# Performance work log

Hardware: AMD Instinct MI355X
Metric: run time of the kernel (lower is better)

## Reference

```python
import jax, jax.numpy as jnp
import numpy as np

# DenoiseTransform(h=10, template_window_size=7, search_window_size=21)
KS = 7                 # odd template window -> kernel_size (7, 7)
SIGMA_COLOR = 10.0     # float(h)
SIGMA_SPACE = 21.0     # float(search_window_size), same for y and x


def _gauss1d(ks, sigma):
    # kornia.get_gaussian_kernel1d: centered, normalized to sum 1
    x = jnp.arange(ks, dtype=jnp.float32) - ks // 2
    g = jnp.exp(-0.5 * (x / sigma) ** 2)
    return g / g.sum()


def setup_inputs() -> dict:
    key = jax.random.key(0)
    # batch of 8 RGB 512x512 images in [0, 1]
    img = jax.random.uniform(key, (8, 3, 512, 512), dtype=jnp.float32)
    return {"img": img}


def reference(img):
    """kornia.filters.bilateral_blur(img, (7,7), 10.0, (21.0,21.0)),
    border_type='reflect', color_distance_type='l1'.
    Fused over the 7x7 window: never materializes (B,C,H,W,49)."""
    ks = KS
    pad = ks // 2
    space = jnp.outer(_gauss1d(ks, SIGMA_SPACE), _gauss1d(ks, SIGMA_SPACE))  # (ks, ks)
    B, C, H, W = img.shape
    padded = jnp.pad(img, ((0, 0), (0, 0), (pad, pad), (pad, pad)), mode="reflect")
    num = jnp.zeros_like(img)                      # (B, C, H, W)
    den = jnp.zeros((B, 1, H, W), dtype=img.dtype)  # (B, 1, H, W)
    neg_half_inv_sc2 = -0.5 / (SIGMA_COLOR ** 2)
    for i in range(ks):          # fixed small 7x7 window -> static unrolled loop
        for j in range(ks):
            patch = jax.lax.dynamic_slice(padded, (0, 0, i, j), (B, C, H, W))
            # L1 color distance over channels, then squared (kornia default 'l1')
            d = jnp.abs(patch - img).sum(axis=1, keepdims=True)  # (B,1,H,W)
            w = space[i, j] * jnp.exp(neg_half_inv_sc2 * d * d)   # (B,1,H,W)
            num = num + w * patch
            den = den + w
    return num / den
```

## Files before the change

### kernel.cpp

```cpp
#include <hip/hip_runtime.h>

#define BB 8
#define HH 512
#define WW 512
#define HW (HH * WW)

typedef float f32x2 __attribute__((ext_vector_type(2)));

__device__ __forceinline__ int reflect512(int v) {
    v = v < 0 ? -v : v;
    return v >= 512 ? 1022 - v : v;
}

__device__ __forceinline__ float swx(int dx) {
    const float SW[7] = {0.98984784f, 0.99547514f, 0.99886688f, 1.0f,
                         0.99886688f, 0.99547514f, 0.98984784f};
    return (dx < -3 || dx > 3) ? 0.0f : SW[dx + 3];
}

#define C1S (-5.0e-3f)
#define C2S (1.25e-5f)

__global__ __launch_bounds__(256) void bilateral_pk2(const float* __restrict__ in,
                                                     float* __restrict__ out) {
    const int blk = blockIdx.x;
    if (blk < BB * HH) {
        const int b = blk >> 9;
        const int y = blk & 511;
        const int p = threadIdx.x;
        if (p >= 253) return;
        const int e  = 4 + 2 * p;
        const int xb = e - 4;

        const float* __restrict__ p0 = in + (size_t)(3 * b) * HW;
        const float* __restrict__ p1 = p0 + HW;
        const float* __restrict__ p2 = p1 + HW;

        const int crow = y * WW;
        f32x2 m0 = *(const f32x2*)(p0 + crow + e - 2);
        f32x2 m1 = *(const f32x2*)(p1 + crow + e - 2);
        f32x2 m2 = *(const f32x2*)(p2 + crow + e - 2);
        f32x2 g0 = *(const f32x2*)(p0 + crow + e);
        f32x2 g1 = *(const f32x2*)(p1 + crow + e);
        f32x2 g2 = *(const f32x2*)(p2 + crow + e);
        const float cA0 = m0.y, cA1 = m1.y, cA2 = m2.y;
        const float cB0 = g0.x, cB1 = g1.x, cB2 = g2.x;

        f32x2 aA0 = {0.f,0.f}, aA1 = {0.f,0.f}, aA2 = {0.f,0.f}, aAd = {0.f,0.f};
        f32x2 aB0 = {0.f,0.f}, aB1 = {0.f,0.f}, aB2 = {0.f,0.f}, aBd = {0.f,0.f};

        const f32x2 C1v = {C1S, C1S};
        const f32x2 C2v = {C2S, C2S};
        const f32x2 ONE = {1.0f, 1.0f};

        #pragma unroll
        for (int j = 0; j < 7; ++j) {
            const float wj = swx(j - 3);
            const int rb = reflect512(y - 3 + j) * WW + xb;
            const float* r0 = p0 + rb;
            const float* r1 = p1 + rb;
            const float* r2 = p2 + rb;
            #pragma unroll
            for (int i = 0; i < 4; ++i) {
                f32x2 q0 = *(const f32x2*)(r0 + 2 * i);
                f32x2 q1 = *(const f32x2*)(r1 + 2 * i);
                f32x2 q2 = *(const f32x2*)(r2 + 2 * i);
                {
                    float dlo = fabsf(q0.x-cA0) + fabsf(q1.x-cA1) + fabsf(q2.x-cA2);
                    float dhi = fabsf(q0.y-cA0) + fabsf(q1.y-cA1) + fabsf(q2.y-cA2);
                    f32x2 dp = {dlo, dhi};
                    f32x2 d2 = dp * dp;
                    const f32x2 sc = {wj * swx(2*i-3), wj * swx(2*i-2)};
                    f32x2 t = C2v * d2 + C1v;
                    f32x2 w = (t * d2 + ONE) * sc;
                    aA0 += w * q0; aA1 += w * q1; aA2 += w * q2; aAd += w;
                }
                {
                    float dlo = fabsf(q0.x-cB0) + fabsf(q1.x-cB1) + fabsf(q2.x-cB2);
                    float dhi = fabsf(q0.y-cB0) + fabsf(q1.y-cB1) + fabsf(q2.y-cB2);
                    f32x2 dp = {dlo, dhi};
                    f32x2 d2 = dp * dp;
                    const f32x2 sc = {wj * swx(2*i-4), wj * swx(2*i-3)};
                    f32x2 t = C2v * d2 + C1v;
                    f32x2 w = (t * d2 + ONE) * sc;
                    aB0 += w * q0; aB1 += w * q1; aB2 += w * q2; aBd += w;
                }
            }
        }

        const float iA = 1.0f / (aAd.x + aAd.y);
        const float iB = 1.0f / (aBd.x + aBd.y);
        size_t ob = (size_t)(3 * b) * HW + crow;
        out[ob + e - 1]          = (aA0.x + aA0.y) * iA;
        out[ob + HW + e - 1]     = (aA1.x + aA1.y) * iA;
        out[ob + 2 * HW + e - 1] = (aA2.x + aA2.y) * iA;
        out[ob + e]              = (aB0.x + aB0.y) * iB;
        out[ob + HW + e]         = (aB1.x + aB1.y) * iB;
        out[ob + 2 * HW + e]     = (aB2.x + aB2.y) * iB;
    } else {
        int idx  = (blk - BB * HH) * 256 + threadIdx.x;
        int ci   = idx % 6;
        int rest = idx / 6;
        int y = rest & 511;
        int b = rest >> 9;
        int x = ci < 3 ? ci : 506 + ci;

        const float* __restrict__ p0 = in + (size_t)(3 * b) * HW;
        const float* __restrict__ p1 = p0 + HW;
        const float* __restrict__ p2 = p1 + HW;
        int cidx = y * WW + x;
        float c0 = p0[cidx], c1 = p1[cidx], c2 = p2[cidx];
        float n0 = 0.f, n1 = 0.f, n2 = 0.f, dn = 0.f;
        #pragma unroll
        for (int dy = 0; dy < 7; ++dy) {
            int rbase = reflect512(y + dy - 3) * WW;
            float wy = swx(dy - 3);
            #pragma unroll
            for (int dx = 0; dx < 7; ++dx) {
                int o = rbase + reflect512(x + dx - 3);
                float q0 = p0[o], q1 = p1[o], q2 = p2[o];
                float d  = fabsf(q0 - c0) + fabsf(q1 - c1) + fabsf(q2 - c2);
                float d2 = d * d;
                float w  = wy * swx(dx - 3) * fmaf(fmaf(C2S, d2, C1S), d2, 1.0f);
                n0 += w * q0; n1 += w * q1; n2 += w * q2; dn += w;
            }
        }
        float inv = 1.0f / dn;
        size_t ob = (size_t)(3 * b) * HW + cidx;
        out[ob] = n0 * inv; out[ob + HW] = n1 * inv; out[ob + 2 * HW] = n2 * inv;
    }
}

extern "C" void kernel_launch(void* const* d_in, const int* in_sizes, int n_in,
                              void* d_out, int out_size, void* d_ws, size_t ws_size,
                              hipStream_t stream) {
    const float* in = (const float*)d_in[0];
    float* out = (float*)d_out;
    int blocks = BB * HH + (BB * HH * 6) / 256;
    bilateral_pk2<<<blocks, 256, 0, stream>>>(in, out);
}
```

Before: 51.04 us.

## Compute two output rows per thread with register row reuse and block swizzle

Each thread now produces a 2x2 output quad (two rows, two columns), so the 8 input rows loaded through a double-buffered register window serve both output rows instead of reloading 7 rows per row. Blocks shrink to 128 threads, each covering half a row-pair, and block indices are swizzled across batches. This cuts global/L2 load traffic per output. In exchange it roughly doubles accumulator register use, which may lower occupancy.

```diff
diff --git a/kernel.cpp b/kernel.cpp
--- a/kernel.cpp
+++ b/kernel.cpp
@@ -21,84 +21,121 @@
 #define C1S (-5.0e-3f)
 #define C2S (1.25e-5f)
 
-__global__ __launch_bounds__(256) void bilateral_pk2(const float* __restrict__ in,
-                                                     float* __restrict__ out) {
+__global__ __launch_bounds__(128) void bilateral_quad(const float* __restrict__ in,
+                                                      float* __restrict__ out) {
     const int blk = blockIdx.x;
-    if (blk < BB * HH) {
-        const int b = blk >> 9;
-        const int y = blk & 511;
-        const int p = threadIdx.x;
-        if (p >= 253) return;
-        const int e  = 4 + 2 * p;
+    if (blk < 4096) {
+        const int swz  = (blk & 7) * 512 + (blk >> 3);
+        const int b    = swz >> 9;
+        const int rest = swz & 511;
+        const int y0   = (rest >> 1) * 2;
+        const int h    = rest & 1;
+        const int p    = threadIdx.x;
+        const int nact = h ? 126 : 127;
+        if (p >= nact) return;
+        const int e  = 4 + 254 * h + 2 * p;
         const int xb = e - 4;
 
         const float* __restrict__ p0 = in + (size_t)(3 * b) * HW;
         const float* __restrict__ p1 = p0 + HW;
         const float* __restrict__ p2 = p1 + HW;
 
-        const int crow = y * WW;
-        f32x2 m0 = *(const f32x2*)(p0 + crow + e - 2);
-        f32x2 m1 = *(const f32x2*)(p1 + crow + e - 2);
-        f32x2 m2 = *(const f32x2*)(p2 + crow + e - 2);
-        f32x2 g0 = *(const f32x2*)(p0 + crow + e);
-        f32x2 g1 = *(const f32x2*)(p1 + crow + e);
-        f32x2 g2 = *(const f32x2*)(p2 + crow + e);
-        const float cA0 = m0.y, cA1 = m1.y, cA2 = m2.y;
-        const float cB0 = g0.x, cB1 = g1.x, cB2 = g2.x;
+        float cA[2][3], cB[2][3];
+        #pragma unroll
+        for (int row = 0; row < 2; ++row) {
+            const int rb = (y0 + row) * WW + xb;
+            f32x2 m0 = *(const f32x2*)(p0 + rb + 2);
+            f32x2 m1 = *(const f32x2*)(p1 + rb + 2);
+            f32x2 m2 = *(const f32x2*)(p2 + rb + 2);
+            f32x2 g0 = *(const f32x2*)(p0 + rb + 4);
+            f32x2 g1 = *(const f32x2*)(p1 + rb + 4);
+            f32x2 g2 = *(const f32x2*)(p2 + rb + 4);
+            cA[row][0] = m0.y; cA[row][1] = m1.y; cA[row][2] = m2.y;
+            cB[row][0] = g0.x; cB[row][1] = g1.x; cB[row][2] = g2.x;
+        }
 
-        f32x2 aA0 = {0.f,0.f}, aA1 = {0.f,0.f}, aA2 = {0.f,0.f}, aAd = {0.f,0.f};
-        f32x2 aB0 = {0.f,0.f}, aB1 = {0.f,0.f}, aB2 = {0.f,0.f}, aBd = {0.f,0.f};
+        f32x2 aN0[2][2], aN1[2][2], aN2[2][2], aD[2][2];
+        #pragma unroll
+        for (int row = 0; row < 2; ++row)
+            #pragma unroll
+            for (int a = 0; a < 2; ++a) {
+                aN0[row][a] = (f32x2){0.f, 0.f}; aN1[row][a] = (f32x2){0.f, 0.f};
+                aN2[row][a] = (f32x2){0.f, 0.f}; aD[row][a]  = (f32x2){0.f, 0.f};
+            }
 
-        const f32x2 C1v = {C1S, C1S};
-        const f32x2 C2v = {C2S, C2S};
-        const f32x2 ONE = {1.0f, 1.0f};
+        f32x2 q0[2][4], q1[2][4], q2[2][4];
+        {
+            const int rb = reflect512(y0 - 3) * WW + xb;
+            #pragma unroll
+            for (int i = 0; i < 4; ++i) {
+                q0[0][i] = *(const f32x2*)(p0 + rb + 2 * i);
+                q1[0][i] = *(const f32x2*)(p1 + rb + 2 * i);
+                q2[0][i] = *(const f32x2*)(p2 + rb + 2 * i);
+            }
+        }
+
+        const f32x2 C1v = {C1S, C1S}, C2v = {C2S, C2S}, ONE = {1.f, 1.f};
 
         #pragma unroll
-        for (int j = 0; j < 7; ++j) {
-            const float wj = swx(j - 3);
-            const int rb = reflect512(y - 3 + j) * WW + xb;
-            const float* r0 = p0 + rb;
-            const float* r1 = p1 + rb;
-            const float* r2 = p2 + rb;
+        for (int r = 0; r < 8; ++r) {
+            const int cur = r & 1, nx = cur ^ 1;
+            if (r < 7) {
+                const int rb = reflect512(y0 - 2 + r) * WW + xb;
+                #pragma unroll
+                for (int i = 0; i < 4; ++i) {
+                    q0[nx][i] = *(const f32x2*)(p0 + rb + 2 * i);
+                    q1[nx][i] = *(const f32x2*)(p1 + rb + 2 * i);
+                    q2[nx][i] = *(const f32x2*)(p2 + rb + 2 * i);
+                }
+            }
             #pragma unroll
             for (int i = 0; i < 4; ++i) {
-                f32x2 q0 = *(const f32x2*)(r0 + 2 * i);
-                f32x2 q1 = *(const f32x2*)(r1 + 2 * i);
-                f32x2 q2 = *(const f32x2*)(r2 + 2 * i);
-                {
-                    float dlo = fabsf(q0.x-cA0) + fabsf(q1.x-cA1) + fabsf(q2.x-cA2);
-                    float dhi = fabsf(q0.y-cA0) + fabsf(q1.y-cA1) + fabsf(q2.y-cA2);
-                    f32x2 dp = {dlo, dhi};
-                    f32x2 d2 = dp * dp;
-                    const f32x2 sc = {wj * swx(2*i-3), wj * swx(2*i-2)};
-                    f32x2 t = C2v * d2 + C1v;
-                    f32x2 w = (t * d2 + ONE) * sc;
-                    aA0 += w * q0; aA1 += w * q1; aA2 += w * q2; aAd += w;
-                }
-                {
-                    float dlo = fabsf(q0.x-cB0) + fabsf(q1.x-cB1) + fabsf(q2.x-cB2);
-                    float dhi = fabsf(q0.y-cB0) + fabsf(q1.y-cB1) + fabsf(q2.y-cB2);
-                    f32x2 dp = {dlo, dhi};
-                    f32x2 d2 = dp * dp;
-                    const f32x2 sc = {wj * swx(2*i-4), wj * swx(2*i-3)};
-                    f32x2 t = C2v * d2 + C1v;
-                    f32x2 w = (t * d2 + ONE) * sc;
-                    aB0 += w * q0; aB1 += w * q1; aB2 += w * q2; aBd += w;
+                const f32x2 v0 = q0[cur][i], v1 = q1[cur][i], v2 = q2[cur][i];
+                #pragma unroll
+                for (int row = 0; row < 2; ++row) {
+                    const int dy = r - row;
+                    if (dy < 0 || dy > 6) continue;
+                    const float wj = swx(dy - 3);
+                    {
+                        float dlo = fabsf(v0.x-cA[row][0]) + fabsf(v1.x-cA[row][1]) + fabsf(v2.x-cA[row][2]);
+                        float dhi = fabsf(v0.y-cA[row][0]) + fabsf(v1.y-cA[row][1]) + fabsf(v2.y-cA[row][2]);
+                        f32x2 dp = {dlo, dhi};
+                        f32x2 d2 = dp * dp;
+                        const f32x2 sc = {wj * swx(2*i-3), wj * swx(2*i-2)};
+                        f32x2 t = C2v * d2 + C1v;
+                        f32x2 w = (t * d2 + ONE) * sc;
+                        aN0[row][0] += w * v0; aN1[row][0] += w * v1;
+                        aN2[row][0] += w * v2; aD[row][0] += w;
+                    }
+                    {
+                        float dlo = fabsf(v0.x-cB[row][0]) + fabsf(v1.x-cB[row][1]) + fabsf(v2.x-cB[row][2]);
+                        float dhi = fabsf(v0.y-cB[row][0]) + fabsf(v1.y-cB[row][1]) + fabsf(v2.y-cB[row][2]);
+                        f32x2 dp = {dlo, dhi};
+                        f32x2 d2 = dp * dp;
+                        const f32x2 sc = {wj * swx(2*i-4), wj * swx(2*i-3)};
+                        f32x2 t = C2v * d2 + C1v;
+                        f32x2 w = (t * d2 + ONE) * sc;
+                        aN0[row][1] += w * v0; aN1[row][1] += w * v1;
+                        aN2[row][1] += w * v2; aD[row][1] += w;
+                    }
                 }
             }
         }
 
-        const float iA = 1.0f / (aAd.x + aAd.y);
-        const float iB = 1.0f / (aBd.x + aBd.y);
-        size_t ob = (size_t)(3 * b) * HW + crow;
-        out[ob + e - 1]          = (aA0.x + aA0.y) * iA;
-        out[ob + HW + e - 1]     = (aA1.x + aA1.y) * iA;
-        out[ob + 2 * HW + e - 1] = (aA2.x + aA2.y) * iA;
-        out[ob + e]              = (aB0.x + aB0.y) * iB;
-        out[ob + HW + e]         = (aB1.x + aB1.y) * iB;
-        out[ob + 2 * HW + e]     = (aB2.x + aB2.y) * iB;
+        #pragma unroll
+        for (int row = 0; row < 2; ++row) {
+            const float iA = 1.0f / (aD[row][0].x + aD[row][0].y);
+            const float iB = 1.0f / (aD[row][1].x + aD[row][1].y);
+            size_t ob = (size_t)(3 * b) * HW + (size_t)(y0 + row) * WW;
+            out[ob + e - 1]          = (aN0[row][0].x + aN0[row][0].y) * iA;
+            out[ob + HW + e - 1]     = (aN1[row][0].x + aN1[row][0].y) * iA;
+            out[ob + 2 * HW + e - 1] = (aN2[row][0].x + aN2[row][0].y) * iA;
+            out[ob + e]              = (aN0[row][1].x + aN0[row][1].y) * iB;
+            out[ob + HW + e]         = (aN1[row][1].x + aN1[row][1].y) * iB;
+            out[ob + 2 * HW + e]     = (aN2[row][1].x + aN2[row][1].y) * iB;
+        }
     } else {
-        int idx  = (blk - BB * HH) * 256 + threadIdx.x;
+        int idx  = (blk - 4096) * 128 + threadIdx.x;
         int ci   = idx % 6;
         int rest = idx / 6;
         int y = rest & 511;
@@ -136,6 +173,6 @@
                               hipStream_t stream) {
     const float* in = (const float*)d_in[0];
     float* out = (float*)d_out;
-    int blocks = BB * HH + (BB * HH * 6) / 256;
-    bilateral_pk2<<<blocks, 256, 0, stream>>>(in, out);
+    int blocks = 4096 + 192;
+    bilateral_quad<<<blocks, 128, 0, stream>>>(in, out);
 }
```

Result: faster. 43.28 us (-15.2%).

## Register-block 4x2 output pixels per thread with shared row loads

Applied to the files above, without the earlier changes.

Each thread now computes a 2-row by 4-column tile of output pixels. It loads 8 input rows as float4 vectors and reuses each loaded row across both output rows and all four columns, which cuts global and L1 load traffic per pixel. The spatial weight is folded into precomputed polynomial coefficients, dropping one multiply per tap. The border path now covers 4 columns on each side. The grid shrinks to 1024+128 blocks, which raises register pressure and may lower occupancy and the number of waves in flight.

```diff
diff --git a/kernel.cpp b/kernel.cpp
--- a/kernel.cpp
+++ b/kernel.cpp
@@ -6,6 +6,7 @@
 #define HW (HH * WW)
 
 typedef float f32x2 __attribute__((ext_vector_type(2)));
+typedef float f32x4 __attribute__((ext_vector_type(4)));
 
 __device__ __forceinline__ int reflect512(int v) {
     v = v < 0 ? -v : v;
@@ -21,89 +22,127 @@
 #define C1S (-5.0e-3f)
 #define C2S (1.25e-5f)
 
-__global__ __launch_bounds__(256) void bilateral_pk2(const float* __restrict__ in,
-                                                     float* __restrict__ out) {
+__global__ __launch_bounds__(256) void bilateral_q8(const float* __restrict__ in,
+                                                    float* __restrict__ out) {
     const int blk = blockIdx.x;
-    if (blk < BB * HH) {
-        const int b = blk >> 9;
-        const int y = blk & 511;
-        const int p = threadIdx.x;
-        if (p >= 253) return;
-        const int e  = 4 + 2 * p;
-        const int xb = e - 4;
+    if (blk < 1024) {
+        const int b   = blk & 7;
+        const int rp2 = blk >> 3;
+        const int sub = threadIdx.x >> 7;
+        const int c   = threadIdx.x & 127;
+        if (c == 0 || c == 127) return;
+        const int y0 = rp2 * 4 + sub * 2;
+        const int x0 = 4 * c;
+        const int xl = x0 - 4;
 
         const float* __restrict__ p0 = in + (size_t)(3 * b) * HW;
         const float* __restrict__ p1 = p0 + HW;
         const float* __restrict__ p2 = p1 + HW;
 
-        const int crow = y * WW;
-        f32x2 m0 = *(const f32x2*)(p0 + crow + e - 2);
-        f32x2 m1 = *(const f32x2*)(p1 + crow + e - 2);
-        f32x2 m2 = *(const f32x2*)(p2 + crow + e - 2);
-        f32x2 g0 = *(const f32x2*)(p0 + crow + e);
-        f32x2 g1 = *(const f32x2*)(p1 + crow + e);
-        f32x2 g2 = *(const f32x2*)(p2 + crow + e);
-        const float cA0 = m0.y, cA1 = m1.y, cA2 = m2.y;
-        const float cB0 = g0.x, cB1 = g1.x, cB2 = g2.x;
+        float cc[2][3][4];
+        #pragma unroll
+        for (int row = 0; row < 2; ++row) {
+            const int cb = (y0 + row) * WW + x0;
+            f32x4 C0 = *(const f32x4*)(p0 + cb);
+            f32x4 C1 = *(const f32x4*)(p1 + cb);
+            f32x4 C2 = *(const f32x4*)(p2 + cb);
+            cc[row][0][0]=C0.x; cc[row][0][1]=C0.y; cc[row][0][2]=C0.z; cc[row][0][3]=C0.w;
+            cc[row][1][0]=C1.x; cc[row][1][1]=C1.y; cc[row][1][2]=C1.z; cc[row][1][3]=C1.w;
+            cc[row][2][0]=C2.x; cc[row][2][1]=C2.y; cc[row][2][2]=C2.z; cc[row][2][3]=C2.w;
+        }
 
-        f32x2 aA0 = {0.f,0.f}, aA1 = {0.f,0.f}, aA2 = {0.f,0.f}, aAd = {0.f,0.f};
-        f32x2 aB0 = {0.f,0.f}, aB1 = {0.f,0.f}, aB2 = {0.f,0.f}, aBd = {0.f,0.f};
+        f32x2 acc[2][4][4];
+        #pragma unroll
+        for (int row = 0; row < 2; ++row)
+            #pragma unroll
+            for (int k = 0; k < 4; ++k)
+                #pragma unroll
+                for (int v = 0; v < 4; ++v) acc[row][k][v] = (f32x2){0.f, 0.f};
 
-        const f32x2 C1v = {C1S, C1S};
-        const f32x2 C2v = {C2S, C2S};
-        const f32x2 ONE = {1.0f, 1.0f};
+        const float SWT[7] = {0.98984784f, 0.99547514f, 0.99886688f, 1.0f,
+                              0.99886688f, 0.99547514f, 0.98984784f};
 
         #pragma unroll
-        for (int j = 0; j < 7; ++j) {
-            const float wj = swx(j - 3);
-            const int rb = reflect512(y - 3 + j) * WW + xb;
-            const float* r0 = p0 + rb;
-            const float* r1 = p1 + rb;
-            const float* r2 = p2 + rb;
+        for (int r = 0; r < 8; ++r) {
+            const int rb = reflect512(y0 - 3 + r) * WW + xl;
+            f32x4 L0a = *(const f32x4*)(p0 + rb);
+            f32x4 L0b = *(const f32x4*)(p0 + rb + 4);
+            f32x4 L0c = *(const f32x4*)(p0 + rb + 8);
+            f32x4 L1a = *(const f32x4*)(p1 + rb);
+            f32x4 L1b = *(const f32x4*)(p1 + rb + 4);
+            f32x4 L1c = *(const f32x4*)(p1 + rb + 8);
+            f32x4 L2a = *(const f32x4*)(p2 + rb);
+            f32x4 L2b = *(const f32x4*)(p2 + rb + 4);
+            f32x4 L2c = *(const f32x4*)(p2 + rb + 8);
+            f32x2 q[6][3];
+            q[0][0]=(f32x2){L0a.x,L0a.y}; q[1][0]=(f32x2){L0a.z,L0a.w};
+            q[2][0]=(f32x2){L0b.x,L0b.y}; q[3][0]=(f32x2){L0b.z,L0b.w};
+            q[4][0]=(f32x2){L0c.x,L0c.y}; q[5][0]=(f32x2){L0c.z,L0c.w};
+            q[0][1]=(f32x2){L1a.x,L1a.y}; q[1][1]=(f32x2){L1a.z,L1a.w};
+            q[2][1]=(f32x2){L1b.x,L1b.y}; q[3][1]=(f32x2){L1b.z,L1b.w};
+            q[4][1]=(f32x2){L1c.x,L1c.y}; q[5][1]=(f32x2){L1c.z,L1c.w};
+            q[0][2]=(f32x2){L2a.x,L2a.y}; q[1][2]=(f32x2){L2a.z,L2a.w};
+            q[2][2]=(f32x2){L2b.x,L2b.y}; q[3][2]=(f32x2){L2b.z,L2b.w};
+            q[4][2]=(f32x2){L2c.x,L2c.y}; q[5][2]=(f32x2){L2c.z,L2c.w};
+
             #pragma unroll
-            for (int i = 0; i < 4; ++i) {
-                f32x2 q0 = *(const f32x2*)(r0 + 2 * i);
-                f32x2 q1 = *(const f32x2*)(r1 + 2 * i);
-                f32x2 q2 = *(const f32x2*)(r2 + 2 * i);
-                {
-                    float dlo = fabsf(q0.x-cA0) + fabsf(q1.x-cA1) + fabsf(q2.x-cA2);
-                    float dhi = fabsf(q0.y-cA0) + fabsf(q1.y-cA1) + fabsf(q2.y-cA2);
-                    f32x2 dp = {dlo, dhi};
-                    f32x2 d2 = dp * dp;
-                    const f32x2 sc = {wj * swx(2*i-3), wj * swx(2*i-2)};
-                    f32x2 t = C2v * d2 + C1v;
-                    f32x2 w = (t * d2 + ONE) * sc;
-                    aA0 += w * q0; aA1 += w * q1; aA2 += w * q2; aAd += w;
-                }
-                {
-                    float dlo = fabsf(q0.x-cB0) + fabsf(q1.x-cB1) + fabsf(q2.x-cB2);
-                    float dhi = fabsf(q0.y-cB0) + fabsf(q1.y-cB1) + fabsf(q2.y-cB2);
-                    f32x2 dp = {dlo, dhi};
-                    f32x2 d2 = dp * dp;
-                    const f32x2 sc = {wj * swx(2*i-4), wj * swx(2*i-3)};
-                    f32x2 t = C2v * d2 + C1v;
-                    f32x2 w = (t * d2 + ONE) * sc;
-                    aB0 += w * q0; aB1 += w * q1; aB2 += w * q2; aBd += w;
+            for (int row = 0; row < 2; ++row) {
+                const int dy = r - row;
+                if (dy < 0 || dy > 6) continue;
+                const float wj = SWT[dy];
+                #pragma unroll
+                for (int k = 0; k < 4; ++k) {
+                    #pragma unroll
+                    for (int P = 0; P < 6; ++P) {
+                        const float wlo = swx(2 * P - 4 - k);
+                        const float whi = swx(2 * P - 3 - k);
+                        if (wlo == 0.f && whi == 0.f) continue;
+                        const f32x2 A2c = {wj * wlo * C2S, wj * whi * C2S};
+                        const f32x2 A1c = {wj * wlo * C1S, wj * whi * C1S};
+                        const f32x2 A0c = {wj * wlo,       wj * whi};
+                        const float k0 = cc[row][0][k], k1 = cc[row][1][k], k2 = cc[row][2][k];
+                        float dlo = fabsf(q[P][0].x - k0) + fabsf(q[P][1].x - k1) +
+                                    fabsf(q[P][2].x - k2);
+                        float dhi = fabsf(q[P][0].y - k0) + fabsf(q[P][1].y - k1) +
+                                    fabsf(q[P][2].y - k2);
+                        f32x2 dp = {dlo, dhi};
+                        f32x2 z  = dp * dp;
+                        f32x2 w  = (A2c * z + A1c) * z + A0c;
+                        acc[row][k][0] += w * q[P][0];
+                        acc[row][k][1] += w * q[P][1];
+                        acc[row][k][2] += w * q[P][2];
+                        acc[row][k][3] += w;
+                    }
                 }
             }
         }
 
-        const float iA = 1.0f / (aAd.x + aAd.y);
-        const float iB = 1.0f / (aBd.x + aBd.y);
-        size_t ob = (size_t)(3 * b) * HW + crow;
-        out[ob + e - 1]          = (aA0.x + aA0.y) * iA;
-        out[ob + HW + e - 1]     = (aA1.x + aA1.y) * iA;
-        out[ob + 2 * HW + e - 1] = (aA2.x + aA2.y) * iA;
-        out[ob + e]              = (aB0.x + aB0.y) * iB;
-        out[ob + HW + e]         = (aB1.x + aB1.y) * iB;
-        out[ob + 2 * HW + e]     = (aB2.x + aB2.y) * iB;
+        #pragma unroll
+        for (int row = 0; row < 2; ++row) {
+            f32x4 o0, o1, o2;
+            #pragma unroll
+            for (int k = 0; k < 4; ++k) {
+                const float inv = 1.0f / (acc[row][k][3].x + acc[row][k][3].y);
+                const float v0 = (acc[row][k][0].x + acc[row][k][0].y) * inv;
+                const float v1 = (acc[row][k][1].x + acc[row][k][1].y) * inv;
+                const float v2 = (acc[row][k][2].x + acc[row][k][2].y) * inv;
+                if (k == 0) { o0.x = v0; o1.x = v1; o2.x = v2; }
+                if (k == 1) { o0.y = v0; o1.y = v1; o2.y = v2; }
+                if (k == 2) { o0.z = v0; o1.z = v1; o2.z = v2; }
+                if (k == 3) { o0.w = v0; o1.w = v1; o2.w = v2; }
+            }
+            size_t ob = (size_t)(3 * b) * HW + (size_t)(y0 + row) * WW + x0;
+            *(f32x4*)(out + ob)          = o0;
+            *(f32x4*)(out + ob + HW)     = o1;
+            *(f32x4*)(out + ob + 2*HW)   = o2;
+        }
     } else {
-        int idx  = (blk - BB * HH) * 256 + threadIdx.x;
-        int ci   = idx % 6;
-        int rest = idx / 6;
+        int idx  = (blk - 1024) * 256 + threadIdx.x;
+        int ci   = idx & 7;
+        int rest = idx >> 3;
         int y = rest & 511;
         int b = rest >> 9;
-        int x = ci < 3 ? ci : 506 + ci;
+        int x = ci < 4 ? ci : 504 + ci;
 
         const float* __restrict__ p0 = in + (size_t)(3 * b) * HW;
         const float* __restrict__ p1 = p0 + HW;
@@ -136,6 +175,6 @@
                               hipStream_t stream) {
     const float* in = (const float*)d_in[0];
     float* out = (float*)d_out;
-    int blocks = BB * HH + (BB * HH * 6) / 256;
-    bilateral_pk2<<<blocks, 256, 0, stream>>>(in, out);
+    int blocks = 1024 + 128;
+    bilateral_q8<<<blocks, 256, 0, stream>>>(in, out);
 }
```

New measurement: 42.76 us (median of 2 runs). 16.2% less time.
